# Kernel optimization log

Measured on AMD Instinct MI355X. Metric: run time of the kernel, lower is better.

Reference implementation:

```python
import jax, jax.numpy as jnp
import numpy as np

N = 100000
E = 3200000
NEG_SLOPE = 0.2


def setup_inputs() -> dict:
    key = jax.random.key(0)
    ks = jax.random.split(key, 12)
    x = jax.random.normal(ks[0], (N, 4), dtype=jnp.float32)
    edge_index = jax.random.randint(ks[1], (2, E), 0, N, dtype=jnp.int64)
    # GATConv(4, 16, heads=4): lin (no bias), att_src/att_dst [H, C], bias [H*C]
    W1 = jax.random.normal(ks[2], (4, 4 * 16), dtype=jnp.float32) * 0.5
    as1 = jax.random.normal(ks[3], (4, 16), dtype=jnp.float32) * 0.5
    ad1 = jax.random.normal(ks[4], (4, 16), dtype=jnp.float32) * 0.5
    b1 = jnp.zeros((64,), dtype=jnp.float32)
    # GATConv(64, 2, heads=4)
    W2 = jax.random.normal(ks[5], (64, 4 * 2), dtype=jnp.float32) * 0.125
    as2 = jax.random.normal(ks[6], (4, 2), dtype=jnp.float32) * 0.5
    ad2 = jax.random.normal(ks[7], (4, 2), dtype=jnp.float32) * 0.5
    b2 = jnp.zeros((8,), dtype=jnp.float32)
    # out head Linear(8, 1)
    Wout = jax.random.normal(ks[8], (8, 1), dtype=jnp.float32) * 0.35
    bout = jnp.zeros((1,), dtype=jnp.float32)
    return {"x": x, "edge_index": edge_index, "W1": W1, "as1": as1, "ad1": ad1,
            "b1": b1, "W2": W2, "as2": as2, "ad2": ad2, "b2": b2,
            "Wout": Wout, "bout": bout}


def gat_conv(x, ei, W, a_src, a_dst, b, H, C, n):
    # PyG GATConv (concat=True, negative_slope=0.2), self-loops already in ei
    xw = (x @ W).reshape(n, H, C)                      # [N, H, C]
    src, dst = ei[0], ei[1]
    alpha_s = jnp.einsum('nhc,hc->nh', xw, a_src)      # [N, H]
    alpha_d = jnp.einsum('nhc,hc->nh', xw, a_dst)      # [N, H]
    e = jax.nn.leaky_relu(alpha_s[src] + alpha_d[dst], NEG_SLOPE)  # [E, H]
    # segment softmax over incoming edges of each destination node
    m = jax.ops.segment_max(e, dst, num_segments=n)    # [N, H]
    e = jnp.exp(e - m[dst])
    denom = jax.ops.segment_sum(e, dst, num_segments=n)
    alpha = e / (denom[dst] + 1e-16)                   # [E, H]
    msg = xw[src] * alpha[:, :, None]                  # [E, H, C]
    out = jax.ops.segment_sum(msg, dst, num_segments=n)  # [N, H, C]
    return out.reshape(n, H * C) + b


def reference(x, edge_index, W1, as1, ad1, b1, W2, as2, ad2, b2, Wout, bout):
    n = x.shape[0]
    ar = jnp.arange(n, dtype=edge_index.dtype)
    ei = jnp.concatenate([edge_index, jnp.stack([ar, ar])], axis=1)  # add self-loops
    h = jax.nn.elu(gat_conv(x, ei, W1, as1, ad1, b1, 4, 16, n))       # [N, 64]
    h = jax.nn.elu(gat_conv(h, ei, W2, as2, ad2, b2, 4, 2, n))        # [N, 8]
    g = jnp.mean(h, axis=0, keepdims=True)  # global_mean_pool, batch all zeros -> [1, 8]
    return jax.nn.sigmoid(g @ Wout + bout)  # [1, 1]
```

## Files before the change

kernel.cpp:

```cpp
#include <hip/hip_runtime.h>
#include <hip/hip_fp8.h>

#define NEG 0.2f
#define BSZ 224
#define MAXBUK 512
#define NBIN 512
#define CAP 16384
#define LSTG 6400
#define LSLAB 11264

typedef float v2f __attribute__((ext_vector_type(2)));

__device__ __forceinline__ float elufast(float x){ return x > 0.0f ? x : __expf(x) - 1.0f; }
__device__ __forceinline__ float b2f(unsigned short b){ return __uint_as_float((unsigned)b << 16); }
__device__ __forceinline__ unsigned short f2b(float x){
    unsigned u = __float_as_uint(x);
    return (unsigned short)((u + 0x7FFFu + ((u >> 16) & 1u)) >> 16);
}

__device__ __forceinline__ void fma8(uint2 r, float w, v2f* acc){
    v2f w2 = {w, w};
    v2f f0 = __builtin_amdgcn_cvt_pk_f32_fp8(r.x, false);
    v2f f1 = __builtin_amdgcn_cvt_pk_f32_fp8(r.x, true);
    v2f f2 = __builtin_amdgcn_cvt_pk_f32_fp8(r.y, false);
    v2f f3 = __builtin_amdgcn_cvt_pk_f32_fp8(r.y, true);
    acc[0] = __builtin_elementwise_fma(f0, w2, acc[0]);
    acc[1] = __builtin_elementwise_fma(f1, w2, acc[1]);
    acc[2] = __builtin_elementwise_fma(f2, w2, acc[2]);
    acc[3] = __builtin_elementwise_fma(f3, w2, acc[3]);
}

__global__ void k_l1_node(const float* __restrict__ x, const float* __restrict__ W1,
                          const float* __restrict__ as1, const float* __restrict__ ad1,
                          unsigned char* __restrict__ xw1, uint2* __restrict__ asvb,
                          float* __restrict__ adv, int N){
    __shared__ float sW[256], sA[64], sD[64];
    int tid = threadIdx.x;
    sW[tid] = W1[tid];
    if (tid < 64){ sA[tid] = as1[tid]; sD[tid] = ad1[tid]; }
    __syncthreads();
    int i = blockIdx.x * 256 + tid;
    if (i >= N) return;
    float4 xv = ((const float4*)x)[i];
    const v2f* sW0 = (const v2f*)sW;
    const v2f* sW1v = (const v2f*)(sW + 64);
    const v2f* sW2v = (const v2f*)(sW + 128);
    const v2f* sW3v = (const v2f*)(sW + 192);
    v2f xx = {xv.x, xv.x}, yy = {xv.y, xv.y}, zz = {xv.z, xv.z}, ww = {xv.w, xv.w};
    v2f xwv[32];
    #pragma unroll
    for (int j = 0; j < 32; j++){
        v2f t = xx * sW0[j];
        t = __builtin_elementwise_fma(yy, sW1v[j], t);
        t = __builtin_elementwise_fma(zz, sW2v[j], t);
        t = __builtin_elementwise_fma(ww, sW3v[j], t);
        xwv[j] = t;
    }
    unsigned wv[16];
    #pragma unroll
    for (int j = 0; j < 16; j++){
        unsigned p = 0;
        p = __builtin_amdgcn_cvt_pk_fp8_f32(xwv[2 * j].x,     xwv[2 * j].y,     p, false);
        p = __builtin_amdgcn_cvt_pk_fp8_f32(xwv[2 * j + 1].x, xwv[2 * j + 1].y, p, true);
        wv[j] = p;
    }
    uint4* dp = (uint4*)(xw1 + (size_t)i * 64);
    dp[0] = make_uint4(wv[0],  wv[1],  wv[2],  wv[3]);
    dp[1] = make_uint4(wv[4],  wv[5],  wv[6],  wv[7]);
    dp[2] = make_uint4(wv[8],  wv[9],  wv[10], wv[11]);
    dp[3] = make_uint4(wv[12], wv[13], wv[14], wv[15]);
    const v2f* sAv = (const v2f*)sA;
    const v2f* sDv = (const v2f*)sD;
    float al[4];
    #pragma unroll
    for (int h = 0; h < 4; h++){
        v2f asv = {0.f, 0.f}, adw = {0.f, 0.f};
        #pragma unroll
        for (int c2 = 0; c2 < 8; c2++){
            asv = __builtin_elementwise_fma(xwv[h * 8 + c2], sAv[h * 8 + c2], asv);
            adw = __builtin_elementwise_fma(xwv[h * 8 + c2], sDv[h * 8 + c2], adw);
        }
        al[h] = asv.x + asv.y;
        adv[i * 4 + h] = adw.x + adw.y;
    }
    asvb[i] = make_uint2((unsigned)f2b(al[0]) | ((unsigned)f2b(al[1]) << 16),
                         (unsigned)f2b(al[2]) | ((unsigned)f2b(al[3]) << 16));
}

__global__ void k_bin2(const int* __restrict__ src, const int* __restrict__ dst,
                       int* __restrict__ gcnt, unsigned* __restrict__ staged,
                       int E, int chunksz, int nbuk){
    __shared__ int histA[MAXBUK], histB[MAXBUK];
    __shared__ int curA[MAXBUK], curB[MAXBUK];
    __shared__ int lsb[MAXBUK];
    __shared__ int gbase[MAXBUK];
    __shared__ int ts[512];
    __shared__ unsigned lstg[LSTG];
    int tid = threadIdx.x;
    int half = tid >> 9;
    int* hist = half ? histB : histA;
    for (int b = tid; b < MAXBUK; b += 1024){ histA[b] = 0; histB[b] = 0; }
    __syncthreads();
    int e0 = blockIdx.x * chunksz, e1 = min(E, e0 + chunksz);
    int a0 = min(e1, (e0 + 3) & ~3);
    int a1 = max(a0, e1 & ~3);
    if (tid < a0 - e0) atomicAdd(&hist[(unsigned)dst[e0 + tid] / BSZ], 1);
    for (int q = (a0 >> 2) + tid; q < (a1 >> 2); q += 1024){
        int4 d4 = ((const int4*)dst)[q];
        atomicAdd(&hist[(unsigned)d4.x / BSZ], 1);
        atomicAdd(&hist[(unsigned)d4.y / BSZ], 1);
        atomicAdd(&hist[(unsigned)d4.z / BSZ], 1);
        atomicAdd(&hist[(unsigned)d4.w / BSZ], 1);
    }
    if (tid < e1 - a1) atomicAdd(&hist[(unsigned)dst[a1 + tid] / BSZ], 1);
    __syncthreads();
    int v = 0, hA = 0;
    if (tid < 512){ hA = histA[tid]; v = hA + histB[tid]; ts[tid] = v; }
    __syncthreads();
    for (int s = 1; s < 512; s <<= 1){
        int tmp = (tid >= s && tid < 512) ? ts[tid - s] : 0;
        __syncthreads();
        if (tid < 512) ts[tid] += tmp;
        __syncthreads();
    }
    if (tid < 512){
        int excl = ts[tid] - v;
        lsb[tid] = excl;
        curA[tid] = excl;
        curB[tid] = excl + hA;
        int padded = (v + 15) & ~15;
        gbase[tid] = tid * CAP + (padded ? atomicAdd(&gcnt[tid], padded) : 0);
    }
    __syncthreads();
    int* cur = half ? curB : curA;
    auto put = [&](int d, int s){
        int buk = (unsigned)d / BSZ;
        int pos = atomicAdd(&cur[buk], 1);
        lstg[pos] = (unsigned)s | ((unsigned)(d - buk * BSZ) << 17);
    };
    if (tid < a0 - e0) put(dst[e0 + tid], src[e0 + tid]);
    for (int q = (a0 >> 2) + tid; q < (a1 >> 2); q += 1024){
        int4 d4 = ((const int4*)dst)[q];
        int4 s4 = ((const int4*)src)[q];
        put(d4.x, s4.x); put(d4.y, s4.y); put(d4.z, s4.z); put(d4.w, s4.w);
    }
    if (tid < e1 - a1) put(dst[a1 + tid], src[a1 + tid]);
    __syncthreads();
    int wv = tid >> 6, ln = tid & 63;
    for (int b = wv; b < nbuk; b += 16){
        int cnt = histA[b] + histB[b];
        int padded = (cnt + 15) & ~15;
        int lb = lsb[b], gb = gbase[b];
        for (int j = ln; j < padded; j += 64)
            staged[gb + j] = (j < cnt) ? lstg[lb + j] : 0xFFFFFFFFu;
    }
}

__global__ void k_local(const unsigned* __restrict__ staged, const int* __restrict__ gcnt,
                        int2* __restrict__ offp, int* __restrict__ csr, int N){
    __shared__ unsigned lslab[LSLAB];
    __shared__ int deg[BSZ];
    __shared__ int cur[BSZ];
    __shared__ int ts[256];
    int b = blockIdx.x, t = threadIdx.x;
    int lo = b * BSZ, hi = min(N, lo + BSZ);
    int e0 = b * CAP;
    int cnt = min(gcnt[b], LSLAB);
    if (t < BSZ) deg[t] = 0;
    __syncthreads();
    for (int q = t; q < (cnt >> 2); q += 1024){
        uint4 s4 = ((const uint4*)(staged + e0))[q];
        ((uint4*)lslab)[q] = s4;
        if (s4.x != 0xFFFFFFFFu) atomicAdd(&deg[s4.x >> 17], 1);
        if (s4.y != 0xFFFFFFFFu) atomicAdd(&deg[s4.y >> 17], 1);
        if (s4.z != 0xFFFFFFFFu) atomicAdd(&deg[s4.z >> 17], 1);
        if (s4.w != 0xFFFFFFFFu) atomicAdd(&deg[s4.w >> 17], 1);
    }
    __syncthreads();
    int v = 0;
    if (t < 256){
        v = (t < BSZ) ? deg[t] : 0;
        ts[t] = v;
    }
    __syncthreads();
    for (int s = 1; s < 256; s <<= 1){
        int tmp = (t >= s && t < 256) ? ts[t - s] : 0;
        __syncthreads();
        if (t < 256) ts[t] += tmp;
        __syncthreads();
    }
    if (t < BSZ){
        cur[t] = e0 + ts[t] - v;
        if (lo + t < hi) offp[lo + t] = make_int2(e0 + ts[t] - v, e0 + ts[t]);
    }
    __syncthreads();
    for (int e = t; e < cnt; e += 1024){
        unsigned se = lslab[e];
        if (se == 0xFFFFFFFFu) continue;
        int pos = atomicAdd(&cur[se >> 17], 1);
        csr[pos] = (int)(se & 0x1FFFFu);
    }
}

__global__ void k_l1_gather(const int2* __restrict__ offp, const int* __restrict__ csr,
                            const uint2* __restrict__ asvb, const float* __restrict__ adv,
                            const unsigned char* __restrict__ xw1, const float* __restrict__ b1,
                            unsigned char* __restrict__ h1f8, int N){
    int tid = threadIdx.x;
    int wid = (int)(((long)blockIdx.x * 256 + tid) >> 6);
    if (wid >= N) return;
    int lane = tid & 63;
    int g = lane >> 3;
    int q = lane & 7;
    int h = q >> 1;
    float advd = adv[wid * 4 + h];
    const unsigned char* xwq = xw1 + q * 8;
    const char* asvbh = (const char*)asvb + h * 2;

    v2f acc2[4] = {{0.f, 0.f}, {0.f, 0.f}, {0.f, 0.f}, {0.f, 0.f}};
    float den = 0.f;
    int2 rng = offp[wid];
    int k = rng.x, end = rng.y;
    for (; k + 32 <= end; k += 32){
        int s0 = csr[k + g];
        int s1 = csr[k + 8 + g];
        int s2 = csr[k + 16 + g];
        int s3 = csr[k + 24 + g];
        uint2 r0 = *(const uint2*)(xwq + ((size_t)s0 << 6));
        uint2 r1 = *(const uint2*)(xwq + ((size_t)s1 << 6));
        uint2 r2 = *(const uint2*)(xwq + ((size_t)s2 << 6));
        uint2 r3 = *(const uint2*)(xwq + ((size_t)s3 << 6));
        float a0 = b2f(*(const unsigned short*)(asvbh + ((size_t)s0 << 3)));
        float a1 = b2f(*(const unsigned short*)(asvbh + ((size_t)s1 << 3)));
        float a2 = b2f(*(const unsigned short*)(asvbh + ((size_t)s2 << 3)));
        float a3 = b2f(*(const unsigned short*)(asvbh + ((size_t)s3 << 3)));
        float t0 = a0 + advd, t1 = a1 + advd, t2 = a2 + advd, t3 = a3 + advd;
        float w0 = __expf(fmaxf(t0, NEG * t0));
        float w1 = __expf(fmaxf(t1, NEG * t1));
        float w2 = __expf(fmaxf(t2, NEG * t2));
        float w3 = __expf(fmaxf(t3, NEG * t3));
        den += (w0 + w1) + (w2 + w3);
        fma8(r0, w0, acc2);
        fma8(r1, w1, acc2);
        fma8(r2, w2, acc2);
        fma8(r3, w3, acc2);
    }
    if (k + 16 <= end){
        int sA = csr[k + g];
        int sB = csr[k + 8 + g];
        uint2 rA = *(const uint2*)(xwq + ((size_t)sA << 6));
        uint2 rB = *(const uint2*)(xwq + ((size_t)sB << 6));
        float aA = b2f(*(const unsigned short*)(asvbh + ((size_t)sA << 3)));
        float aB = b2f(*(const unsigned short*)(asvbh + ((size_t)sB << 3)));
        float tA = aA + advd, tB = aB + advd;
        float wA = __expf(fmaxf(tA, NEG * tA));
        float wB = __expf(fmaxf(tB, NEG * tB));
        den += wA + wB;
        fma8(rA, wA, acc2);
        fma8(rB, wB, acc2);
        k += 16;
    }
    for (; k < end; k += 8){
        int e = k + g;
        bool valid = e < end;
        int s = csr[valid ? e : end - 1];
        uint2 r = *(const uint2*)(xwq + ((size_t)s << 6));
        float a = b2f(*(const unsigned short*)(asvbh + ((size_t)s << 3)));
        float t = a + advd;
        float w = valid ? __expf(fmaxf(t, NEG * t)) : 0.f;
        den += w;
        fma8(r, w, acc2);
    }

    v2f t0, t1, t2, t3;
    t0.x = __shfl_xor(acc2[0].x, 32); t0.y = __shfl_xor(acc2[0].y, 32);
    t1.x = __shfl_xor(acc2[1].x, 32); t1.y = __shfl_xor(acc2[1].y, 32);
    t2.x = __shfl_xor(acc2[2].x, 32); t2.y = __shfl_xor(acc2[2].y, 32);
    t3.x = __shfl_xor(acc2[3].x, 32); t3.y = __shfl_xor(acc2[3].y, 32);
    bool gb2 = (lane & 32) != 0;
    v2f n0 = gb2 ? (acc2[2] + t2) : (acc2[0] + t0);
    v2f n1 = gb2 ? (acc2[3] + t3) : (acc2[1] + t1);
    v2f u0, u1;
    u0.x = __shfl_xor(n0.x, 16); u0.y = __shfl_xor(n0.y, 16);
    u1.x = __shfl_xor(n1.x, 16); u1.y = __shfl_xor(n1.y, 16);
    bool gb1 = (lane & 16) != 0;
    v2f rr = gb1 ? (n1 + u1) : (n0 + u0);
    v2f z;
    z.x = __shfl_xor(rr.x, 8); z.y = __shfl_xor(rr.y, 8);
    rr += z;
    bool gb0 = (lane & 8) != 0;
    den += __shfl_xor(den, 8);
    den += __shfl_xor(den, 16);
    den += __shfl_xor(den, 32);
    float val = gb0 ? rr.y : rr.x;

    int c = q * 8 + g;
    float aself = b2f(*(const unsigned short*)(asvbh + ((size_t)wid << 3)));
    float tsv = aself + advd;
    float ws = __expf(fmaxf(tsv, NEG * tsv));
    unsigned selfb = xw1[(size_t)wid * 64 + c];
    v2f sf = __builtin_amdgcn_cvt_pk_f32_fp8(selfb, false);
    float asel = val + ws * sf.x;
    float inv = 1.0f / (den + ws + 1e-16f);
    float o = elufast(asel * inv + b1[c]);
    unsigned p = __builtin_amdgcn_cvt_pk_fp8_f32(o, o, 0, false);
    h1f8[(size_t)wid * 64 + c] = (unsigned char)p;
}

__global__ void k_l2_node(const unsigned char* __restrict__ h1f8, const float* __restrict__ W2,
                          const float* __restrict__ ad2, float* __restrict__ xw2,
                          float* __restrict__ adv2, int N){
    __shared__ float sW[512], sD[8];
    int tid = threadIdx.x;
    sW[tid] = W2[tid];
    sW[256 + tid] = W2[256 + tid];
    if (tid < 8) sD[tid] = ad2[tid];
    __syncthreads();
    int i = blockIdx.x * 256 + tid;
    if (i >= N) return;
    const uint2* rp = (const uint2*)(h1f8 + (size_t)i * 64);
    v2f acc2[4] = {{0.f, 0.f}, {0.f, 0.f}, {0.f, 0.f}, {0.f, 0.f}};
    #pragma unroll
    for (int b8 = 0; b8 < 8; b8++){
        uint2 r = rp[b8];
        v2f f0 = __builtin_amdgcn_cvt_pk_f32_fp8(r.x, false);
        v2f f1 = __builtin_amdgcn_cvt_pk_f32_fp8(r.x, true);
        v2f f2 = __builtin_amdgcn_cvt_pk_f32_fp8(r.y, false);
        v2f f3 = __builtin_amdgcn_cvt_pk_f32_fp8(r.y, true);
        float f[8] = {f0.x, f0.y, f1.x, f1.y, f2.x, f2.y, f3.x, f3.y};
        #pragma unroll
        for (int j = 0; j < 8; j++){
            v2f hcv = {f[j], f[j]};
            const v2f* wrow = (const v2f*)&sW[(b8 * 8 + j) * 8];
            acc2[0] = __builtin_elementwise_fma(hcv, wrow[0], acc2[0]);
            acc2[1] = __builtin_elementwise_fma(hcv, wrow[1], acc2[1]);
            acc2[2] = __builtin_elementwise_fma(hcv, wrow[2], acc2[2]);
            acc2[3] = __builtin_elementwise_fma(hcv, wrow[3], acc2[3]);
        }
    }
    float4* xo = (float4*)(xw2 + (size_t)i * 8);
    xo[0] = make_float4(acc2[0].x, acc2[0].y, acc2[1].x, acc2[1].y);
    xo[1] = make_float4(acc2[2].x, acc2[2].y, acc2[3].x, acc2[3].y);
    float4 dv;
    dv.x = acc2[0].x * sD[0] + acc2[0].y * sD[1];
    dv.y = acc2[1].x * sD[2] + acc2[1].y * sD[3];
    dv.z = acc2[2].x * sD[4] + acc2[2].y * sD[5];
    dv.w = acc2[3].x * sD[6] + acc2[3].y * sD[7];
    *(float4*)(adv2 + (size_t)i * 4) = dv;
}

__global__ void k_l2_gather(const int2* __restrict__ offp, const int* __restrict__ csr,
                            const float* __restrict__ adv2, const float* __restrict__ xw2,
                            const float* __restrict__ b2, const float* __restrict__ as2,
                            float* __restrict__ pool, int N){
    __shared__ float lpool[8];
    int tid = threadIdx.x;
    if (tid < 8) lpool[tid] = 0.f;
    __syncthreads();
    int wid = (int)(((long)blockIdx.x * 256 + tid) >> 6);
    if (wid < N){
        int lane = tid & 63;
        int g = lane >> 2;
        int hh = lane & 3;
        float2 a2h = *(const float2*)&as2[hh * 2];
        float advd = adv2[wid * 4 + hh];
        const char* xwh = (const char*)xw2 + hh * 8;
        v2f accv = {0.f, 0.f};
        float den = 0.f;

        auto edge = [&](int s, bool valid){
            v2f v = *(const v2f*)(xwh + ((size_t)s << 5));
            float al = v.x * a2h.x + v.y * a2h.y;
            float t = al + advd;
            float w = valid ? __expf(fmaxf(t, NEG * t)) : 0.f;
            den += w;
            v2f w2 = {w, w};
            accv = __builtin_elementwise_fma(v, w2, accv);
        };

        int2 rng = offp[wid];
        int k = rng.x, end = rng.y;
        for (; k + 32 <= end; k += 32){
            int s0 = csr[k + g], s1 = csr[k + 16 + g];
            edge(s0, true); edge(s1, true);
        }
        for (; k < end; k += 16){
            int e = k + g;
            bool valid = e < end;
            int s = csr[valid ? e : end - 1];
            edge(s, valid);
        }
        #pragma unroll
        for (int m = 4; m <= 32; m <<= 1){
            accv.x += __shfl_xor(accv.x, m);
            accv.y += __shfl_xor(accv.y, m);
            den    += __shfl_xor(den, m);
        }
        if (g == 0){
            v2f v = *(const v2f*)(xwh + ((size_t)wid << 5));
            float al = v.x * a2h.x + v.y * a2h.y;
            float t = al + advd;
            float ws = __expf(fmaxf(t, NEG * t));
            den += ws;
            accv.x += ws * v.x;
            accv.y += ws * v.y;
            float inv = 1.0f / (den + 1e-16f);
            float o0 = elufast(accv.x * inv + b2[hh * 2]);
            float o1 = elufast(accv.y * inv + b2[hh * 2 + 1]);
            atomicAdd(&lpool[hh * 2], o0);
            atomicAdd(&lpool[hh * 2 + 1], o1);
        }
    }
    __syncthreads();
    if (tid < 8) atomicAdd(&pool[(blockIdx.x & 63) * 8 + tid], lpool[tid]);
}

__global__ void k_final(const float* __restrict__ pool, const float* __restrict__ Wout,
                        const float* __restrict__ bout, float* __restrict__ out, float invN){
    int lane = threadIdx.x;
    const float4* p4 = (const float4*)(pool + lane * 8);
    float4 a = p4[0], b = p4[1];
    float v[8] = {a.x, a.y, a.z, a.w, b.x, b.y, b.z, b.w};
    #pragma unroll
    for (int m = 1; m <= 32; m <<= 1){
        #pragma unroll
        for (int j = 0; j < 8; j++) v[j] += __shfl_xor(v[j], m);
    }
    if (lane == 0){
        float z = bout[0];
        #pragma unroll
        for (int j = 0; j < 8; j++) z += v[j] * invN * Wout[j];
        out[0] = 1.0f / (1.0f + __expf(-z));
    }
}

extern "C" void kernel_launch(void* const* d_in, const int* in_sizes, int n_in,
                              void* d_out, int out_size, void* d_ws, size_t ws_size,
                              hipStream_t stream){
    const float* x    = (const float*)d_in[0];
    const int*   ei   = (const int*)d_in[1];
    const float* W1   = (const float*)d_in[2];
    const float* as1  = (const float*)d_in[3];
    const float* ad1  = (const float*)d_in[4];
    const float* b1   = (const float*)d_in[5];
    const float* W2   = (const float*)d_in[6];
    const float* as2  = (const float*)d_in[7];
    const float* ad2  = (const float*)d_in[8];
    const float* b2   = (const float*)d_in[9];
    const float* Wout = (const float*)d_in[10];
    const float* bout = (const float*)d_in[11];
    float* out = (float*)d_out;

    int N = in_sizes[0] / 4;
    int E = in_sizes[1] / 2;
    const int* src = ei;
    const int* dst = ei + E;

    char* ws = (char*)d_ws;
    size_t off_b = 0;
    auto alloc = [&](size_t bytes)->void*{
        void* p = ws + off_b;
        off_b += (bytes + 255) & ~(size_t)255;
        return p;
    };
    unsigned char* xw1  = (unsigned char*)alloc((size_t)N * 64);
    unsigned char* h1f8 = (unsigned char*)alloc((size_t)N * 64);
    uint2*    asvb   = (uint2*)alloc((size_t)N * 8);
    float*    adv    = (float*)alloc((size_t)N * 4 * 4);
    float*    adv2   = (float*)alloc((size_t)N * 4 * 4);
    int*      gcnt   = (int*)alloc((size_t)MAXBUK * 4);
    unsigned* staged = (unsigned*)alloc((size_t)MAXBUK * CAP * 4);
    int2*     offp   = (int2*)alloc((size_t)N * 8);
    int*      csr    = (int*)alloc((size_t)MAXBUK * CAP * 4);
    float*    xw2    = (float*)alloc((size_t)N * 8 * 4);
    float*    pool   = (float*)alloc(64 * 8 * 4);

    int nbuk = (N + BSZ - 1) / BSZ;
    int chunksz = (E + NBIN - 1) / NBIN;

    hipMemsetAsync(pool, 0, 64 * 8 * 4, stream);
    hipMemsetAsync(gcnt, 0, (size_t)MAXBUK * 4, stream);

    k_bin2<<<NBIN, 1024, 0, stream>>>(src, dst, gcnt, staged, E, chunksz, nbuk);
    k_l1_node<<<(N + 255) / 256, 256, 0, stream>>>(x, W1, as1, ad1, xw1, asvb, adv, N);
    k_local<<<nbuk, 1024, 0, stream>>>(staged, gcnt, offp, csr, N);

    k_l1_gather<<<(int)(((long)N * 64 + 255) / 256), 256, 0, stream>>>(
        offp, csr, asvb, adv, xw1, b1, h1f8, N);
    k_l2_node<<<(N + 255) / 256, 256, 0, stream>>>(h1f8, W2, ad2, xw2, adv2, N);
    k_l2_gather<<<(int)(((long)N * 64 + 255) / 256), 256, 0, stream>>>(
        offp, csr, adv2, xw2, b2, as2, pool, N);
    k_final<<<1, 64, 0, stream>>>(pool, Wout, bout, out, 1.0f / (float)N);
}
```

Before: 161.5 us.

## Fuse layer-1 node transform into edge binning kernel as interleaved blocks

Merges the layer-1 node projection kernel into the edge binning kernel by adding extra blocks to one grid. Node blocks are spread evenly among the binning blocks and each handles 512 nodes, two threads per node, each computing half the channels and heads. This removes one kernel launch and lets the node transform overlap with the atomic-heavy binning work. In exchange, node blocks carry the binning kernel's large shared-memory footprint and 1024-thread shape, which may limit occupancy.

```diff
diff --git a/kernel.cpp b/kernel.cpp
--- a/kernel.cpp
+++ b/kernel.cpp
@@ -30,78 +30,86 @@
     acc[3] = __builtin_elementwise_fma(f3, w2, acc[3]);
 }
 
-__global__ void k_l1_node(const float* __restrict__ x, const float* __restrict__ W1,
-                          const float* __restrict__ as1, const float* __restrict__ ad1,
-                          unsigned char* __restrict__ xw1, uint2* __restrict__ asvb,
-                          float* __restrict__ adv, int N){
-    __shared__ float sW[256], sA[64], sD[64];
-    int tid = threadIdx.x;
-    sW[tid] = W1[tid];
-    if (tid < 64){ sA[tid] = as1[tid]; sD[tid] = ad1[tid]; }
-    __syncthreads();
-    int i = blockIdx.x * 256 + tid;
-    if (i >= N) return;
-    float4 xv = ((const float4*)x)[i];
-    const v2f* sW0 = (const v2f*)sW;
-    const v2f* sW1v = (const v2f*)(sW + 64);
-    const v2f* sW2v = (const v2f*)(sW + 128);
-    const v2f* sW3v = (const v2f*)(sW + 192);
-    v2f xx = {xv.x, xv.x}, yy = {xv.y, xv.y}, zz = {xv.z, xv.z}, ww = {xv.w, xv.w};
-    v2f xwv[32];
-    #pragma unroll
-    for (int j = 0; j < 32; j++){
-        v2f t = xx * sW0[j];
-        t = __builtin_elementwise_fma(yy, sW1v[j], t);
-        t = __builtin_elementwise_fma(zz, sW2v[j], t);
-        t = __builtin_elementwise_fma(ww, sW3v[j], t);
-        xwv[j] = t;
-    }
-    unsigned wv[16];
-    #pragma unroll
-    for (int j = 0; j < 16; j++){
-        unsigned p = 0;
-        p = __builtin_amdgcn_cvt_pk_fp8_f32(xwv[2 * j].x,     xwv[2 * j].y,     p, false);
-        p = __builtin_amdgcn_cvt_pk_fp8_f32(xwv[2 * j + 1].x, xwv[2 * j + 1].y, p, true);
-        wv[j] = p;
-    }
-    uint4* dp = (uint4*)(xw1 + (size_t)i * 64);
-    dp[0] = make_uint4(wv[0],  wv[1],  wv[2],  wv[3]);
-    dp[1] = make_uint4(wv[4],  wv[5],  wv[6],  wv[7]);
-    dp[2] = make_uint4(wv[8],  wv[9],  wv[10], wv[11]);
-    dp[3] = make_uint4(wv[12], wv[13], wv[14], wv[15]);
-    const v2f* sAv = (const v2f*)sA;
-    const v2f* sDv = (const v2f*)sD;
-    float al[4];
-    #pragma unroll
-    for (int h = 0; h < 4; h++){
-        v2f asv = {0.f, 0.f}, adw = {0.f, 0.f};
-        #pragma unroll
-        for (int c2 = 0; c2 < 8; c2++){
-            asv = __builtin_elementwise_fma(xwv[h * 8 + c2], sAv[h * 8 + c2], asv);
-            adw = __builtin_elementwise_fma(xwv[h * 8 + c2], sDv[h * 8 + c2], adw);
-        }
-        al[h] = asv.x + asv.y;
-        adv[i * 4 + h] = adw.x + adw.y;
-    }
-    asvb[i] = make_uint2((unsigned)f2b(al[0]) | ((unsigned)f2b(al[1]) << 16),
-                         (unsigned)f2b(al[2]) | ((unsigned)f2b(al[3]) << 16));
-}
-
-__global__ void k_bin2(const int* __restrict__ src, const int* __restrict__ dst,
-                       int* __restrict__ gcnt, unsigned* __restrict__ staged,
-                       int E, int chunksz, int nbuk){
+__global__ __launch_bounds__(1024, 8)
+void k_bin_node(const int* __restrict__ src, const int* __restrict__ dst,
+                int* __restrict__ gcnt, unsigned* __restrict__ staged,
+                const float* __restrict__ x, const float* __restrict__ W1,
+                const float* __restrict__ as1, const float* __restrict__ ad1,
+                unsigned char* __restrict__ xw1, unsigned* __restrict__ asvb32,
+                float* __restrict__ adv,
+                int E, int chunksz, int nbuk, int N, int nnodeblk, int grid){
     __shared__ int histA[MAXBUK], histB[MAXBUK];
     __shared__ int curA[MAXBUK], curB[MAXBUK];
     __shared__ int lsb[MAXBUK];
     __shared__ int gbase[MAXBUK];
     __shared__ int ts[512];
     __shared__ unsigned lstg[LSTG];
+    __shared__ float sW[256], sA[64], sD[64];
+    int r = blockIdx.x;
+    int nodeBefore = (int)(((long)r * nnodeblk) / grid);
+    int isNode = (int)(((long)(r + 1) * nnodeblk) / grid) > nodeBefore;
     int tid = threadIdx.x;
+
+    if (isNode){
+        if (tid < 256) sW[tid] = W1[tid];
+        else if (tid < 320) sA[tid - 256] = as1[tid - 256];
+        else if (tid < 384) sD[tid - 320] = ad1[tid - 320];
+        __syncthreads();
+        int half = tid & 1;
+        int i = nodeBefore * 512 + (tid >> 1);
+        if (i >= N) return;
+        float4 xv = ((const float4*)x)[i];
+        const v2f* r0 = (const v2f*)(sW      ) + half * 16;
+        const v2f* r1 = (const v2f*)(sW + 64 ) + half * 16;
+        const v2f* r2 = (const v2f*)(sW + 128) + half * 16;
+        const v2f* r3 = (const v2f*)(sW + 192) + half * 16;
+        v2f xx = {xv.x, xv.x}, yy = {xv.y, xv.y}, zz = {xv.z, xv.z}, ww = {xv.w, xv.w};
+        v2f xwv[16];
+        #pragma unroll
+        for (int j = 0; j < 16; j++){
+            v2f t = xx * r0[j];
+            t = __builtin_elementwise_fma(yy, r1[j], t);
+            t = __builtin_elementwise_fma(zz, r2[j], t);
+            t = __builtin_elementwise_fma(ww, r3[j], t);
+            xwv[j] = t;
+        }
+        unsigned wv[8];
+        #pragma unroll
+        for (int j = 0; j < 8; j++){
+            unsigned p = 0;
+            p = __builtin_amdgcn_cvt_pk_fp8_f32(xwv[2 * j].x,     xwv[2 * j].y,     p, false);
+            p = __builtin_amdgcn_cvt_pk_fp8_f32(xwv[2 * j + 1].x, xwv[2 * j + 1].y, p, true);
+            wv[j] = p;
+        }
+        uint4* dp = (uint4*)(xw1 + (size_t)i * 64 + half * 32);
+        dp[0] = make_uint4(wv[0], wv[1], wv[2], wv[3]);
+        dp[1] = make_uint4(wv[4], wv[5], wv[6], wv[7]);
+        const v2f* sAv = (const v2f*)sA + half * 16;
+        const v2f* sDv = (const v2f*)sD + half * 16;
+        float al[2], ad_[2];
+        #pragma unroll
+        for (int hh = 0; hh < 2; hh++){
+            v2f asv = {0.f, 0.f}, adw = {0.f, 0.f};
+            #pragma unroll
+            for (int c2 = 0; c2 < 8; c2++){
+                asv = __builtin_elementwise_fma(xwv[hh * 8 + c2], sAv[hh * 8 + c2], asv);
+                adw = __builtin_elementwise_fma(xwv[hh * 8 + c2], sDv[hh * 8 + c2], adw);
+            }
+            al[hh] = asv.x + asv.y;
+            ad_[hh] = adw.x + adw.y;
+        }
+        asvb32[(size_t)i * 2 + half] = (unsigned)f2b(al[0]) | ((unsigned)f2b(al[1]) << 16);
+        float2 adpair = {ad_[0], ad_[1]};
+        *(float2*)(adv + (size_t)i * 4 + half * 2) = adpair;
+        return;
+    }
+
+    int bid = r - nodeBefore;
     int half = tid >> 9;
     int* hist = half ? histB : histA;
     for (int b = tid; b < MAXBUK; b += 1024){ histA[b] = 0; histB[b] = 0; }
     __syncthreads();
-    int e0 = blockIdx.x * chunksz, e1 = min(E, e0 + chunksz);
+    int e0 = bid * chunksz, e1 = min(E, e0 + chunksz);
     int a0 = min(e1, (e0 + 3) & ~3);
     int a1 = max(a0, e1 & ~3);
     if (tid < a0 - e0) atomicAdd(&hist[(unsigned)dst[e0 + tid] / BSZ], 1);
@@ -146,8 +154,8 @@
     }
     if (tid < e1 - a1) put(dst[a1 + tid], src[a1 + tid]);
     __syncthreads();
-    int wv = tid >> 6, ln = tid & 63;
-    for (int b = wv; b < nbuk; b += 16){
+    int wvi = tid >> 6, ln = tid & 63;
+    for (int b = wvi; b < nbuk; b += 16){
         int cnt = histA[b] + histB[b];
         int padded = (cnt + 15) & ~15;
         int lb = lsb[b], gb = gbase[b];
@@ -477,12 +485,15 @@
 
     int nbuk = (N + BSZ - 1) / BSZ;
     int chunksz = (E + NBIN - 1) / NBIN;
+    int nnodeblk = (N + 511) / 512;
+    int grid = NBIN + nnodeblk;
 
     hipMemsetAsync(pool, 0, 64 * 8 * 4, stream);
     hipMemsetAsync(gcnt, 0, (size_t)MAXBUK * 4, stream);
 
-    k_bin2<<<NBIN, 1024, 0, stream>>>(src, dst, gcnt, staged, E, chunksz, nbuk);
-    k_l1_node<<<(N + 255) / 256, 256, 0, stream>>>(x, W1, as1, ad1, xw1, asvb, adv, N);
+    k_bin_node<<<grid, 1024, 0, stream>>>(src, dst, gcnt, staged,
+                                          x, W1, as1, ad1, xw1, (unsigned*)asvb, adv,
+                                          E, chunksz, nbuk, N, nnodeblk, grid);
     k_local<<<nbuk, 1024, 0, stream>>>(staged, gcnt, offp, csr, N);
 
     k_l1_gather<<<(int)(((long)N * 64 + 255) / 256), 256, 0, stream>>>(
```

Measured after the change: 160.6 us. About the same (-0.6%).
